# Kernel optimization log

Hardware: AMD Instinct MI355X
Metric: run time of the kernel (lower is better)

## Reference

```python
import jax, jax.numpy as jnp
import numpy as np

B, C, P = 512, 202, 27          # batch, n_band (200 hyper + superpixel + train/test), patch size
CH = C - 2                      # hyper channels fed to conv
N = P * P                       # flattened patch
K = int(N * 0.08)
OUTC = 64


def setup_inputs() -> dict:
    key = jax.random.key(0)
    k1, k2, k3, k4, k5 = jax.random.split(key, 5)
    x = jax.random.normal(k1, (B, C, P, P), jnp.float32)
    # superpixel channel: small positive integer labels (avoid 0, which the original handles buggily)
    sp = jax.random.randint(k2, (B, P, P), 1, 21).astype(jnp.float32)
    x = x.at[:, C - 2].set(sp)
    # per-batch random flat indices without replacement (np.random.choice equivalent)
    perm = jax.vmap(lambda k: jax.random.permutation(k, N))(jax.random.split(k3, B))
    rand_idx = perm[:, :K].astype(jnp.int32)
    W = jax.random.normal(k4, (OUTC, CH, 3, 3), jnp.float32) * 0.05
    b = jax.random.normal(k5, (OUTC,), jnp.float32) * 0.05
    return {"x": x, "W": W, "b": b, "rand_idx": rand_idx}


def reference(x, W, b, rand_idx):
    # original detaches the image before the superpixel gather/scatter
    xd = jax.lax.stop_gradient(x)
    img = jnp.transpose(xd, (0, 2, 3, 1))            # [B,P,P,C]
    hyper = img[..., :CH].reshape(B, N, CH)          # [B,N,CH]
    sp = img[..., CH].reshape(B, N)                  # superpixel labels [B,N]
    central = img[:, P // 2, P // 2, CH]             # [B]
    brow = jnp.arange(B)[:, None]
    sp = sp.at[brow, rand_idx].set(jnp.broadcast_to(central[:, None], (B, K)))
    mask = sp == central[:, None]                    # True where pixel belongs to central superpixel
    # zero-pixel k (row-major) sources from one-pixel (k mod num_one) -- tiling semantics of original
    zrank = jnp.cumsum((~mask).astype(jnp.int32), axis=1) - 1   # rank among zeros
    num_one = mask.sum(axis=1)                                  # >= 1 (center pixel)
    order = jnp.argsort(jnp.where(mask, 0, 1), axis=1)          # stable: one-positions first, row-major
    src = jnp.take_along_axis(order, zrank % num_one[:, None], axis=1)  # [B,N]
    gathered = jnp.take_along_axis(hyper, src[..., None], axis=1)       # [B,N,CH]
    out = jnp.where(mask[..., None], hyper, gathered).reshape(B, P, P, CH)
    x_off = jnp.transpose(out, (0, 3, 1, 2))         # [B,CH,P,P]
    y = jax.lax.conv_general_dilated(x_off, W, (1, 1), 'SAME')
    return y + b[None, :, None, None]
```

## Files before the change

### kernel.cpp

```cpp
#include <hip/hip_runtime.h>

#define Bn 512
#define Cn 202
#define Pn 27
#define Nn 729
#define CHn 200
#define Kn 58
#define OUTCn 64
#define CENTERn 364
#define NCHUNK 7
#define POOLR 128
#define ZSLOT 127
#define NCK8 28
#define MCAP 128
#define SPAD 864
#define WTOT (NCHUNK * 9 * OUTCn * 32)
#define UST 20

typedef float f32x4 __attribute__((ext_vector_type(4)));
typedef f32x4 f32x4u __attribute__((aligned(4)));
typedef short s16x8 __attribute__((ext_vector_type(8)));
typedef short s16x4 __attribute__((ext_vector_type(4)));

static __device__ __forceinline__ unsigned short f2bf(float f) {
  unsigned u = __float_as_uint(f);
  u += 0x7fffu + ((u >> 16) & 1u);
  return (unsigned short)(u >> 16);
}
static __device__ __forceinline__ float bf2f(short s) {
  return __uint_as_float(((unsigned)(unsigned short)s) << 16);
}

__global__ __launch_bounds__(256) void src_kernel(const float* __restrict__ x,
                                                  const int* __restrict__ rand_idx,
                                                  const float* __restrict__ W,
                                                  short* __restrict__ slotpad_ws,
                                                  short* __restrict__ Mws,
                                                  int* __restrict__ num1_ws,
                                                  short* __restrict__ Wt2) {
  int b = blockIdx.x;
  __shared__ float sp[Nn];
  __shared__ short slotS[Nn];
  __shared__ short M[Nn];
  __shared__ int wsum[4];
  __shared__ int s_num;
  int tid = threadIdx.x;
  const int lane = tid & 63;
  const int wv = tid >> 6;
  const float* xsp = x + ((size_t)b * Cn + CHn) * Nn;
  for (int n = tid; n < Nn; n += 256) sp[n] = xsp[n];
  __syncthreads();
  float central = sp[CENTERn];
  __syncthreads();
  for (int k = tid; k < Kn; k += 256) sp[rand_idx[b * Kn + k]] = central;
  __syncthreads();

  int n0 = tid * 3;
  bool mk[3];
  int cnt = 0;
#pragma unroll
  for (int t = 0; t < 3; ++t) {
    int n = n0 + t;
    bool m = (n < Nn) && (sp[n] == central);
    mk[t] = m;
    cnt += m;
  }
  int v = cnt;
#pragma unroll
  for (int off = 1; off < 64; off <<= 1) {
    int u = __shfl_up(v, off);
    if (lane >= off) v += u;
  }
  if (lane == 63) wsum[wv] = v;
  __syncthreads();
  if (tid == 0) {
    int s = 0;
#pragma unroll
    for (int w = 0; w < 4; ++w) { int t = wsum[w]; wsum[w] = s; s += t; }
    s_num = s;
  }
  __syncthreads();
  int num = s_num;
  int excl = v - cnt + wsum[wv];
  int c = excl;
#pragma unroll
  for (int t = 0; t < 3; ++t) {
    int n = n0 + t;
    if (n < Nn) {
      if (mk[t]) { M[c] = (short)n; slotS[n] = (short)c; c++; }
      else { slotS[n] = (short)(~(n - c)); }
    }
  }
  __syncthreads();

  int num1 = num < ZSLOT ? num : ZSLOT;
  if (tid == 0) num1_ws[b] = num1;
  for (int m = tid; m < MCAP; m += 256) Mws[(size_t)b * MCAP + m] = (m < num) ? M[m] : (short)0;
  for (int idx = tid; idx < 841; idx += 256) {
    int pi = idx / 29, pj = idx - pi * 29;
    short val = (short)ZSLOT;
    if (pi >= 1 && pi <= 27 && pj >= 1 && pj <= 27) {
      int n = (pi - 1) * Pn + (pj - 1);
      int s0 = slotS[n];
      int sv = (s0 >= 0) ? s0 : ((~s0) % num);
      if (sv > ZSLOT - 1) sv = ZSLOT - 1;
      val = (short)sv;
    }
    slotpad_ws[(size_t)b * SPAD + idx] = val;
  }

  if (tid < 252) {
    int idx = b * 252 + tid;
    int ck = idx / (9 * OUTCn * 32);
    int rem = idx - ck * (9 * OUTCn * 32);
    int r = rem / (OUTCn * 32);
    int rem2 = rem - r * (OUTCn * 32);
    int o = rem2 >> 5;
    int cl = rem2 & 31;
    int cc = ck * 32 + cl;
    float wval = (cc < CHn) ? W[((size_t)o * CHn + cc) * 9 + r] : 0.f;
    Wt2[idx] = (short)f2bf(wval);
  }
}

__global__ __launch_bounds__(256) void pool_kernel(const float* __restrict__ x,
                                                   const short* __restrict__ Mws,
                                                   const int* __restrict__ num1_ws,
                                                   short* __restrict__ Pool_ws) {
  __shared__ __align__(16) float xs[8 * Nn];
  const int ck8 = blockIdx.x;
  const int b = blockIdx.y;
  const int tid = threadIdx.x;
  const int c0 = ck8 * 8;
  const float* xp = x + ((size_t)b * Cn + c0) * Nn;

  const f32x4u* xp4 = (const f32x4u*)xp;
  f32x4* xs4 = (f32x4*)xs;
  for (int v = tid; v < (8 * Nn) / 4; v += 256) xs4[v] = xp4[v];
  __syncthreads();

  if (tid < POOLR) {
    const int m = tid;
    const int num1 = num1_ws[b];
    bool valid = m < num1;
    int s = valid ? (int)Mws[(size_t)b * MCAP + m] : 0;
    s16x8 w8;
#pragma unroll
    for (int j = 0; j < 8; ++j) {
      float v = valid ? xs[j * Nn + s] : 0.f;
      w8[j] = (short)f2bf(v);
    }
    *(s16x8*)(Pool_ws + ((size_t)b * NCK8 + ck8) * (POOLR * 8) + m * 8) = w8;
  }
}

__global__ __launch_bounds__(512) void fused2_kernel(const short* __restrict__ Wt2,
                                                     const short* __restrict__ Pool_ws,
                                                     const float* __restrict__ bias,
                                                     const short* __restrict__ slotpad_ws,
                                                     float* __restrict__ y) {
  __shared__ short Slot[841];
  __shared__ __align__(16) short Ulds[9 * POOLR * UST];
  const int q = blockIdx.x;
  const int b = blockIdx.y;
  const int tid = threadIdx.x;
  const int lane = tid & 63;
  const int wv = tid >> 6;
  const int l16 = lane & 15;
  const int kg = lane >> 4;

  for (int i2 = tid; i2 < 841; i2 += 512) Slot[i2] = slotpad_ws[(size_t)b * SPAD + i2];

  {
    const short* poolb = Pool_ws + (size_t)b * (NCK8 * POOLR * 8);
    s16x8 bv[NCHUNK];
#pragma unroll
    for (int ck = 0; ck < NCHUNK; ++ck)
      bv[ck] = *(const s16x8*)(poolb + ((size_t)(ck * 4 + kg) * POOLR + wv * 16 + l16) * 8);
#pragma unroll
    for (int r = 0; r < 9; ++r) {
      const short* wp = Wt2 + ((size_t)r * OUTCn + q * 16 + l16) * 32 + kg * 8;
      f32x4 a = (f32x4){0.f, 0.f, 0.f, 0.f};
#pragma unroll
      for (int ck = 0; ck < NCHUNK; ++ck) {
        s16x8 av = *(const s16x8*)(wp + (size_t)ck * (9 * OUTCn * 32));
        a = __builtin_amdgcn_mfma_f32_16x16x32_bf16(av, bv[ck], a, 0, 0, 0);
      }
      s16x4 u4 = {(short)f2bf(a[0]), (short)f2bf(a[1]), (short)f2bf(a[2]), (short)f2bf(a[3])};
      *(s16x4*)(Ulds + ((size_t)r * POOLR + wv * 16 + l16) * UST + kg * 4) = u4;
    }
  }
  __syncthreads();

  float accA[16], accB[16];
#pragma unroll
  for (int j = 0; j < 16; ++j) { accA[j] = 0.f; accB[j] = 0.f; }

  const int n1 = tid;
  const int pi1 = n1 / Pn, pj1 = n1 - pi1 * Pn;
  const int base1 = pi1 * 29 + pj1;
  const bool has2 = (tid + 512) < Nn;
  const int n2 = has2 ? (tid + 512) : n1;
  const int pi2 = n2 / Pn, pj2 = n2 - pi2 * Pn;
  const int base2 = pi2 * 29 + pj2;

#pragma unroll
  for (int r = 0; r < 9; ++r) {
    const int off = (r / 3) * 29 + (r % 3);
    {
      int slot = Slot[base1 + off];
      const short* u = Ulds + ((size_t)r * POOLR + slot) * UST;
#pragma unroll
      for (int seg = 0; seg < 4; ++seg) {
        s16x4 v = *(const s16x4*)(u + seg * 4);
        accA[seg * 4 + 0] += bf2f(v[0]);
        accA[seg * 4 + 1] += bf2f(v[1]);
        accA[seg * 4 + 2] += bf2f(v[2]);
        accA[seg * 4 + 3] += bf2f(v[3]);
      }
    }
    if (has2) {
      int slot = Slot[base2 + off];
      const short* u = Ulds + ((size_t)r * POOLR + slot) * UST;
#pragma unroll
      for (int seg = 0; seg < 4; ++seg) {
        s16x4 v = *(const s16x4*)(u + seg * 4);
        accB[seg * 4 + 0] += bf2f(v[0]);
        accB[seg * 4 + 1] += bf2f(v[1]);
        accB[seg * 4 + 2] += bf2f(v[2]);
        accB[seg * 4 + 3] += bf2f(v[3]);
      }
    }
  }

  float* yb = y + ((size_t)b * OUTCn + q * 16) * Nn;
#pragma unroll
  for (int j = 0; j < 16; ++j) {
    float bo = bias[q * 16 + j];
    yb[(size_t)j * Nn + n1] = accA[j] + bo;
    if (has2) yb[(size_t)j * Nn + n2] = accB[j] + bo;
  }
}

extern "C" void kernel_launch(void* const* d_in, const int* in_sizes, int n_in,
                              void* d_out, int out_size, void* d_ws, size_t ws_size,
                              hipStream_t stream) {
  const float* x = (const float*)d_in[0];
  const float* W = (const float*)d_in[1];
  const float* bias = (const float*)d_in[2];
  const int* rand_idx = (const int*)d_in[3];
  float* y = (float*)d_out;

  char* p = (char*)d_ws;
  short* slotpad = (short*)p;   p += (size_t)Bn * SPAD * 2;
  short* Mws = (short*)p;       p += (size_t)Bn * MCAP * 2;
  int* num1 = (int*)p;          p += 2048;
  short* Wt2 = (short*)p;       p += (size_t)WTOT * 2;
  short* Pool_ws = (short*)p;

  src_kernel<<<Bn, 256, 0, stream>>>(x, rand_idx, W, slotpad, Mws, num1, Wt2);
  pool_kernel<<<dim3(25, Bn), 256, 0, stream>>>(x, Mws, num1, Pool_ws);
  fused2_kernel<<<dim3(4, Bn), 512, 0, stream>>>(Wt2, Pool_ws, bias, slotpad, y);
}
```

Measured before the change: 154.0 us.

## Fuse source-index and pool kernels into one prep kernel

Merges the per-batch superpixel mask/scan kernel with the channel-pooling gather kernel. Each pool block recomputes the mask and prefix scan locally, and one extra block per batch writes the slot map and weight transform. This removes a kernel launch, the inter-kernel dependency and the Mws/num1 workspace round trip. The cost is that the scan is repeated 26 times per batch and shared memory per block grows, which may lower occupancy.

```diff
diff --git a/kernel.cpp b/kernel.cpp
--- a/kernel.cpp
+++ b/kernel.cpp
@@ -12,7 +12,6 @@
 #define POOLR 128
 #define ZSLOT 127
 #define NCK8 28
-#define MCAP 128
 #define SPAD 864
 #define WTOT (NCHUNK * 9 * OUTCn * 32)
 #define UST 20
@@ -31,24 +30,34 @@
   return __uint_as_float(((unsigned)(unsigned short)s) << 16);
 }
 
-__global__ __launch_bounds__(256) void src_kernel(const float* __restrict__ x,
-                                                  const int* __restrict__ rand_idx,
-                                                  const float* __restrict__ W,
-                                                  short* __restrict__ slotpad_ws,
-                                                  short* __restrict__ Mws,
-                                                  int* __restrict__ num1_ws,
-                                                  short* __restrict__ Wt2) {
-  int b = blockIdx.x;
+__global__ __launch_bounds__(256) void prep_kernel(const float* __restrict__ x,
+                                                   const int* __restrict__ rand_idx,
+                                                   const float* __restrict__ W,
+                                                   short* __restrict__ slotpad_ws,
+                                                   short* __restrict__ Wt2,
+                                                   short* __restrict__ Pool_ws) {
   __shared__ float sp[Nn];
+  __shared__ short M[Nn];
   __shared__ short slotS[Nn];
-  __shared__ short M[Nn];
   __shared__ int wsum[4];
   __shared__ int s_num;
-  int tid = threadIdx.x;
+  __shared__ __align__(16) float xs[8 * Nn];
+
+  const int ck8 = blockIdx.x;
+  const int b = blockIdx.y;
+  const int tid = threadIdx.x;
   const int lane = tid & 63;
   const int wv = tid >> 6;
+  const bool is_pool = ck8 < 25;
+
   const float* xsp = x + ((size_t)b * Cn + CHn) * Nn;
   for (int n = tid; n < Nn; n += 256) sp[n] = xsp[n];
+  if (is_pool) {
+    const float* xp = x + ((size_t)b * Cn + ck8 * 8) * Nn;
+    const f32x4u* xp4 = (const f32x4u*)xp;
+    f32x4* xs4 = (f32x4*)xs;
+    for (int v = tid; v < (8 * Nn) / 4; v += 256) xs4[v] = xp4[v];
+  }
   __syncthreads();
   float central = sp[CENTERn];
   __syncthreads();
@@ -93,64 +102,45 @@
   }
   __syncthreads();
 
-  int num1 = num < ZSLOT ? num : ZSLOT;
-  if (tid == 0) num1_ws[b] = num1;
-  for (int m = tid; m < MCAP; m += 256) Mws[(size_t)b * MCAP + m] = (m < num) ? M[m] : (short)0;
-  for (int idx = tid; idx < 841; idx += 256) {
-    int pi = idx / 29, pj = idx - pi * 29;
-    short val = (short)ZSLOT;
-    if (pi >= 1 && pi <= 27 && pj >= 1 && pj <= 27) {
-      int n = (pi - 1) * Pn + (pj - 1);
-      int s0 = slotS[n];
-      int sv = (s0 >= 0) ? s0 : ((~s0) % num);
-      if (sv > ZSLOT - 1) sv = ZSLOT - 1;
-      val = (short)sv;
-    }
-    slotpad_ws[(size_t)b * SPAD + idx] = val;
-  }
-
-  if (tid < 252) {
-    int idx = b * 252 + tid;
-    int ck = idx / (9 * OUTCn * 32);
-    int rem = idx - ck * (9 * OUTCn * 32);
-    int r = rem / (OUTCn * 32);
-    int rem2 = rem - r * (OUTCn * 32);
-    int o = rem2 >> 5;
-    int cl = rem2 & 31;
-    int cc = ck * 32 + cl;
-    float wval = (cc < CHn) ? W[((size_t)o * CHn + cc) * 9 + r] : 0.f;
-    Wt2[idx] = (short)f2bf(wval);
-  }
-}
-
-__global__ __launch_bounds__(256) void pool_kernel(const float* __restrict__ x,
-                                                   const short* __restrict__ Mws,
-                                                   const int* __restrict__ num1_ws,
-                                                   short* __restrict__ Pool_ws) {
-  __shared__ __align__(16) float xs[8 * Nn];
-  const int ck8 = blockIdx.x;
-  const int b = blockIdx.y;
-  const int tid = threadIdx.x;
-  const int c0 = ck8 * 8;
-  const float* xp = x + ((size_t)b * Cn + c0) * Nn;
-
-  const f32x4u* xp4 = (const f32x4u*)xp;
-  f32x4* xs4 = (f32x4*)xs;
-  for (int v = tid; v < (8 * Nn) / 4; v += 256) xs4[v] = xp4[v];
-  __syncthreads();
-
-  if (tid < POOLR) {
-    const int m = tid;
-    const int num1 = num1_ws[b];
-    bool valid = m < num1;
-    int s = valid ? (int)Mws[(size_t)b * MCAP + m] : 0;
-    s16x8 w8;
-#pragma unroll
-    for (int j = 0; j < 8; ++j) {
-      float v = valid ? xs[j * Nn + s] : 0.f;
-      w8[j] = (short)f2bf(v);
-    }
-    *(s16x8*)(Pool_ws + ((size_t)b * NCK8 + ck8) * (POOLR * 8) + m * 8) = w8;
+  if (is_pool) {
+    if (tid < POOLR) {
+      const int m = tid;
+      const int num1 = num < ZSLOT ? num : ZSLOT;
+      bool valid = m < num1;
+      int s = valid ? (int)M[m] : 0;
+      s16x8 w8;
+#pragma unroll
+      for (int j = 0; j < 8; ++j) {
+        float fv = valid ? xs[j * Nn + s] : 0.f;
+        w8[j] = (short)f2bf(fv);
+      }
+      *(s16x8*)(Pool_ws + ((size_t)b * NCK8 + ck8) * (POOLR * 8) + m * 8) = w8;
+    }
+  } else {
+    for (int idx = tid; idx < 841; idx += 256) {
+      int pi = idx / 29, pj = idx - pi * 29;
+      short val = (short)ZSLOT;
+      if (pi >= 1 && pi <= 27 && pj >= 1 && pj <= 27) {
+        int n = (pi - 1) * Pn + (pj - 1);
+        int s0 = slotS[n];
+        int sv = (s0 >= 0) ? s0 : ((~s0) % num);
+        if (sv > ZSLOT - 1) sv = ZSLOT - 1;
+        val = (short)sv;
+      }
+      slotpad_ws[(size_t)b * SPAD + idx] = val;
+    }
+    if (tid < 252) {
+      int idx = b * 252 + tid;
+      int ck = idx / (9 * OUTCn * 32);
+      int rem = idx - ck * (9 * OUTCn * 32);
+      int r = rem / (OUTCn * 32);
+      int rem2 = rem - r * (OUTCn * 32);
+      int o = rem2 >> 5;
+      int cl = rem2 & 31;
+      int cc = ck * 32 + cl;
+      float wval = (cc < CHn) ? W[((size_t)o * CHn + cc) * 9 + r] : 0.f;
+      Wt2[idx] = (short)f2bf(wval);
+    }
   }
 }
 
@@ -212,11 +202,11 @@
       const short* u = Ulds + ((size_t)r * POOLR + slot) * UST;
 #pragma unroll
       for (int seg = 0; seg < 4; ++seg) {
-        s16x4 v = *(const s16x4*)(u + seg * 4);
-        accA[seg * 4 + 0] += bf2f(v[0]);
-        accA[seg * 4 + 1] += bf2f(v[1]);
-        accA[seg * 4 + 2] += bf2f(v[2]);
-        accA[seg * 4 + 3] += bf2f(v[3]);
+        s16x4 vv = *(const s16x4*)(u + seg * 4);
+        accA[seg * 4 + 0] += bf2f(vv[0]);
+        accA[seg * 4 + 1] += bf2f(vv[1]);
+        accA[seg * 4 + 2] += bf2f(vv[2]);
+        accA[seg * 4 + 3] += bf2f(vv[3]);
       }
     }
     if (has2) {
@@ -224,11 +214,11 @@
       const short* u = Ulds + ((size_t)r * POOLR + slot) * UST;
 #pragma unroll
       for (int seg = 0; seg < 4; ++seg) {
-        s16x4 v = *(const s16x4*)(u + seg * 4);
-        accB[seg * 4 + 0] += bf2f(v[0]);
-        accB[seg * 4 + 1] += bf2f(v[1]);
-        accB[seg * 4 + 2] += bf2f(v[2]);
-        accB[seg * 4 + 3] += bf2f(v[3]);
+        s16x4 vv = *(const s16x4*)(u + seg * 4);
+        accB[seg * 4 + 0] += bf2f(vv[0]);
+        accB[seg * 4 + 1] += bf2f(vv[1]);
+        accB[seg * 4 + 2] += bf2f(vv[2]);
+        accB[seg * 4 + 3] += bf2f(vv[3]);
       }
     }
   }
@@ -253,12 +243,9 @@
 
   char* p = (char*)d_ws;
   short* slotpad = (short*)p;   p += (size_t)Bn * SPAD * 2;
-  short* Mws = (short*)p;       p += (size_t)Bn * MCAP * 2;
-  int* num1 = (int*)p;          p += 2048;
   short* Wt2 = (short*)p;       p += (size_t)WTOT * 2;
   short* Pool_ws = (short*)p;
 
-  src_kernel<<<Bn, 256, 0, stream>>>(x, rand_idx, W, slotpad, Mws, num1, Wt2);
-  pool_kernel<<<dim3(25, Bn), 256, 0, stream>>>(x, Mws, num1, Pool_ws);
+  prep_kernel<<<dim3(26, Bn), 256, 0, stream>>>(x, rand_idx, W, slotpad, Wt2, Pool_ws);
   fused2_kernel<<<dim3(4, Bn), 512, 0, stream>>>(Wt2, Pool_ws, bias, slotpad, y);
 }
```

Result: slower. 168.0 us (+9.1%).
